# Kernel optimization log

Hardware: AMD Instinct MI355X
Metric: run time of the kernel (lower is better)

## Reference

```python
import jax, jax.numpy as jnp
import numpy as np

N_NODES = 100000
N_EDGES = 3200000
N_GRAPHS = 512
F_IN = 256
HID = 16
N_CLS = 8


def setup_inputs() -> dict:
    key = jax.random.key(0)
    ks = jax.random.split(key, 6)
    x = jax.random.normal(ks[0], (N_NODES, F_IN), jnp.float32)
    edge_index = jax.random.randint(ks[1], (2, N_EDGES), 0, N_NODES, dtype=jnp.int64)
    batch = jnp.sort(jax.random.randint(ks[2], (N_NODES,), 0, N_GRAPHS, dtype=jnp.int64))
    W1 = jax.random.normal(ks[3], (F_IN, HID), jnp.float32) / np.float32(np.sqrt(F_IN))
    b1 = jnp.zeros((HID,), jnp.float32)
    W2 = jax.random.normal(ks[4], (HID, N_CLS), jnp.float32) / np.float32(np.sqrt(HID))
    b2 = jnp.zeros((N_CLS,), jnp.float32)
    return {"x": x, "edge_index": edge_index, "batch": batch, "num_graphs": N_GRAPHS,
            "W1": W1, "b1": b1, "W2": W2, "b2": b2}


def _gcn_conv(x, src, dst, W, b, n):
    # PyG GCNConv: linear transform, then sym-normalized scatter-add (self-loops
    # already appended to src/dst by caller), bias added after aggregation.
    h = x @ W  # [N, out]
    deg = jax.ops.segment_sum(jnp.ones_like(dst, h.dtype), dst, num_segments=n)
    dinv = jax.lax.rsqrt(jnp.maximum(deg, 1.0))  # deg >= 1 due to self-loops
    norm = dinv[src] * dinv[dst]  # [E+N]
    out = jax.ops.segment_sum(h[src] * norm[:, None], dst, num_segments=n)
    return out + b


def reference(x, edge_index, batch, num_graphs, W1, b1, W2, b2):
    n = x.shape[0]
    loop = jnp.arange(n, dtype=edge_index.dtype)
    src = jnp.concatenate([edge_index[0], loop])
    dst = jnp.concatenate([edge_index[1], loop])
    h = jax.nn.relu(_gcn_conv(x, src, dst, W1, b1, n))
    h = _gcn_conv(h, src, dst, W2, b2, n)
    # global mean pool over graphs
    sums = jax.ops.segment_sum(h, batch, num_segments=num_graphs)
    cnt = jax.ops.segment_sum(jnp.ones((n,), h.dtype), batch, num_segments=num_graphs)
    return sums / jnp.maximum(cnt, 1.0)[:, None]
```

## Files before the change

kernel.cpp:

```cpp
#include <hip/hip_runtime.h>

#define F_IN 256
#define HID 16
#define NCLS 8
#define BSH 9
#define NPB 512
#define MAXBINS 256
#define BCAP 18432u
#define TILE 8192
#define WIN 8
#define GROWS 64
#define APITCH 280
#define BSPLIT 4

typedef float f4v __attribute__((ext_vector_type(4)));
typedef float f32x4 __attribute__((ext_vector_type(4)));
typedef _Float16 h2v __attribute__((ext_vector_type(2)));
typedef _Float16 f16x4 __attribute__((ext_vector_type(4)));
typedef _Float16 f16x8 __attribute__((ext_vector_type(8)));

__global__ void k_init(unsigned* __restrict__ binCur, int nbins,
                       const float* __restrict__ W1, _Float16* __restrict__ wfrag,
                       float* __restrict__ cg, int g,
                       float* __restrict__ out, int osz) {
    int t = threadIdx.x;
    if (t < nbins) binCur[t] = (unsigned)t * BCAP;
    if (t < 64) {
        int col = t & 15, k0 = (t >> 4) * 8;
#pragma unroll
        for (int kc = 0; kc < 8; ++kc) {
            f16x8 v;
#pragma unroll
            for (int j = 0; j < 8; ++j)
                v[j] = (_Float16)W1[(kc * 32 + k0 + j) * HID + col];
            *(f16x8*)&wfrag[((size_t)t * 8 + kc) * 8] = v;
        }
    }
    for (int i = t; i < g; i += 256) cg[i] = 0.f;
    for (int i = t; i < osz; i += 256) out[i] = 0.f;
}

__global__ void __launch_bounds__(512) k_binA(const int* __restrict__ src,
                                              const int* __restrict__ dst, int e,
                                              unsigned* __restrict__ binCur,
                                              unsigned* __restrict__ binbuf) {
    __shared__ unsigned scnt[MAXBINS], lbase[MAXBINS], gbase[MAXBINS];
    __shared__ unsigned sbuf[TILE];
    __shared__ unsigned char sbin[TILE];
    int t = threadIdx.x;
    if (t < MAXBINS) scnt[t] = 0u;
    __syncthreads();
    int base = blockIdx.x * TILE;
    unsigned ent[16], rank[16];
    int ebin[16];
#pragma unroll
    for (int i = 0; i < 16; ++i) {
        int j = base + t + i * 512;
        ebin[i] = -1;
        if (j < e) {
            int d = __builtin_nontemporal_load(&dst[j]);
            int s = __builtin_nontemporal_load(&src[j]);
            ent[i] = ((unsigned)s << BSH) | ((unsigned)d & (NPB - 1));
            ebin[i] = d >> BSH;
            rank[i] = atomicAdd(&scnt[ebin[i]], 1u);
        }
    }
    __syncthreads();
    if (t == 0) {
        unsigned run = 0;
        for (int b = 0; b < MAXBINS; ++b) { lbase[b] = run; run += scnt[b]; }
    }
    __syncthreads();
    if (t < MAXBINS && scnt[t] > 0u) gbase[t] = atomicAdd(&binCur[t], scnt[t]);
    __syncthreads();
#pragma unroll
    for (int i = 0; i < 16; ++i)
        if (ebin[i] >= 0) {
            unsigned p = lbase[ebin[i]] + rank[i];
            sbuf[p] = ent[i];
            sbin[p] = (unsigned char)ebin[i];
        }
    __syncthreads();
    int total = e - base; if (total > TILE) total = TILE;
    for (int idx = t; idx < total; idx += 512) {
        int b = sbin[idx];
        __builtin_nontemporal_store(sbuf[idx], &binbuf[gbase[b] + ((unsigned)idx - lbase[b])]);
    }
}

__global__ void __launch_bounds__(256) k_binB1(const unsigned* __restrict__ binbuf,
                                               const unsigned* __restrict__ binCur,
                                               unsigned* __restrict__ phist) {
    __shared__ unsigned hist[NPB];
    int t = threadIdx.x;
    int b = blockIdx.x >> 2, sp = blockIdx.x & 3;
    unsigned base = (unsigned)b * BCAP;
    unsigned cnt = binCur[b] - base;
    unsigned q = cnt / BSPLIT;
    unsigned j0 = sp * q, j1 = (sp == BSPLIT - 1) ? cnt : j0 + q;
    for (int i = t; i < NPB; i += 256) hist[i] = 0u;
    __syncthreads();
    for (unsigned j = j0 + t; j < j1; j += 256)
        atomicAdd(&hist[__builtin_nontemporal_load(&binbuf[base + j]) & (NPB - 1)], 1u);
    __syncthreads();
    unsigned* ph = phist + ((size_t)b * BSPLIT + sp) * NPB;
    for (int i = t; i < NPB; i += 256) ph[i] = hist[i];
}

__global__ void __launch_bounds__(256) k_binB2(unsigned* __restrict__ phist, int n,
                                               unsigned* __restrict__ off,
                                               unsigned* __restrict__ degc) {
    __shared__ unsigned deg[NPB];
    __shared__ unsigned pref[NPB];
    __shared__ unsigned s1[256];
    int t = threadIdx.x;
    int b = blockIdx.x;
    unsigned* ph = phist + (size_t)b * BSPLIT * NPB;
    for (int i = t; i < NPB; i += 256) {
        unsigned c0 = ph[i], c1 = ph[NPB + i], c2 = ph[2 * NPB + i], c3 = ph[3 * NPB + i];
        ph[i] = 0u; ph[NPB + i] = c0; ph[2 * NPB + i] = c0 + c1; ph[3 * NPB + i] = c0 + c1 + c2;
        deg[i] = c0 + c1 + c2 + c3;
    }
    __syncthreads();
    unsigned h0 = deg[2 * t], h1 = deg[2 * t + 1];
    unsigned pair = h0 + h1;
    s1[t] = pair;
    __syncthreads();
    for (int o = 1; o < 256; o <<= 1) {
        unsigned v = (t >= o) ? s1[t - o] : 0u;
        __syncthreads();
        s1[t] += v;
        __syncthreads();
    }
    unsigned exc = s1[t] - pair;
    pref[2 * t] = exc;
    pref[2 * t + 1] = exc + h0;
    __syncthreads();
    unsigned base = (unsigned)b * BCAP;
    int dbase = b << BSH;
    for (int i = t; i < NPB; i += 256) {
        int d = dbase + i;
        if (d < n) { off[d] = base + pref[i]; degc[d] = deg[i]; }
    }
}

__global__ void __launch_bounds__(256) k_binB3(const unsigned* __restrict__ binbuf,
                                               const unsigned* __restrict__ binCur,
                                               const unsigned* __restrict__ phist,
                                               const unsigned* __restrict__ off,
                                               int n, unsigned* __restrict__ srcs) {
    __shared__ unsigned cst[NPB], cur[NPB], offl[NPB];
    int t = threadIdx.x;
    int b = blockIdx.x >> 2, sp = blockIdx.x & 3;
    unsigned base = (unsigned)b * BCAP;
    unsigned cnt = binCur[b] - base;
    unsigned q = cnt / BSPLIT;
    unsigned j0 = sp * q, j1 = (sp == BSPLIT - 1) ? cnt : j0 + q;
    const unsigned* ph = phist + ((size_t)b * BSPLIT + sp) * NPB;
    int dbase = b << BSH;
    for (int i = t; i < NPB; i += 256) {
        cst[i] = ph[i];
        cur[i] = 0u;
        int d = dbase + i;
        offl[i] = (d < n) ? off[d] : 0u;
    }
    __syncthreads();
    for (unsigned j = j0 + t; j < j1; j += 256) {
        unsigned v = __builtin_nontemporal_load(&binbuf[base + j]);
        unsigned dl = v & (NPB - 1);
        unsigned r = atomicAdd(&cur[dl], 1u);
        srcs[offl[dl] + cst[dl] + r] = v >> BSH;
    }
}

__global__ void __launch_bounds__(256) k_gemm1(const float* __restrict__ x,
                                               const _Float16* __restrict__ wfrag,
                                               const unsigned* __restrict__ degc,
                                               _Float16* __restrict__ t1h, int n) {
    __shared__ _Float16 xs[4][16 * APITCH];
    int t = threadIdx.x;
    int lane = t & 63;
    int wv = t >> 6;
    int col = lane & 15;
    int k0 = (lane >> 4) * 8;
    f16x8 bfrag[8];
#pragma unroll
    for (int kc = 0; kc < 8; ++kc)
        bfrag[kc] = *(const f16x8*)&wfrag[((size_t)lane * 8 + kc) * 8];
    int rbase = blockIdx.x * GROWS;
    int nrows = n - rbase; if (nrows > GROWS) nrows = GROWS;
#pragma unroll
    for (int it = 0; it < GROWS * 64 / 256; ++it) {
        int q = t + it * 256;
        int row = q >> 6, c4 = q & 63;
        if (row < nrows) {
            f4v v = __builtin_nontemporal_load(
                &((const f4v*)(x + (size_t)(rbase + row) * F_IN))[c4]);
            f16x4 hv;
            hv[0] = (_Float16)v[0]; hv[1] = (_Float16)v[1];
            hv[2] = (_Float16)v[2]; hv[3] = (_Float16)v[3];
            *(f16x4*)&xs[row >> 4][(row & 15) * APITCH + c4 * 4] = hv;
        }
    }
    __syncthreads();
    f32x4 acc = {0.f, 0.f, 0.f, 0.f};
    const _Float16* tile = xs[wv];
    int arow = lane & 15;
#pragma unroll
    for (int kc = 0; kc < 8; ++kc) {
        f16x8 afrag = *(const f16x8*)&tile[arow * APITCH + kc * 32 + k0];
        acc = __builtin_amdgcn_mfma_f32_16x16x32_f16(afrag, bfrag[kc], acc, 0, 0, 0);
    }
    int r0 = (lane >> 4) * 4;
#pragma unroll
    for (int reg = 0; reg < 4; ++reg) {
        int grow = rbase + wv * 16 + r0 + reg;
        if (grow < n) {
            float v = acc[reg] * rsqrtf((float)(degc[grow] + 1u));
            t1h[(size_t)grow * HID + col] = (_Float16)v;
        }
    }
}

__global__ void __launch_bounds__(256) k_agg1g2(const unsigned* __restrict__ srcs,
                                                const unsigned* __restrict__ off,
                                                const unsigned* __restrict__ degc,
                                                const uint2* __restrict__ t1q,
                                                const float* __restrict__ b1,
                                                const float* __restrict__ W2,
                                                unsigned* __restrict__ t2h, int n) {
    __shared__ float w2s[HID * NCLS];
    __shared__ float b1s[HID];
    int t = threadIdx.x;
    if (t < HID * NCLS) w2s[t] = W2[t];
    if (t < HID) b1s[t] = b1[t];
    __syncthreads();
    int d = blockIdx.x * 32 + (t >> 3);
    if (d >= n) return;
    int q4 = t & 3;
    int pr = (t >> 2) & 1;
    unsigned p = off[d];
    unsigned c = degc[d];
    float a0 = 0.f, a1 = 0.f, a2 = 0.f, a3 = 0.f;
    union { unsigned u; h2v h; } cv;
    unsigned i = pr;
    for (; i + 14 < c; i += 16) {
        unsigned s0 = srcs[p + i],      s1 = srcs[p + i + 2];
        unsigned s2 = srcs[p + i + 4],  s3 = srcs[p + i + 6];
        unsigned s4 = srcs[p + i + 8],  s5 = srcs[p + i + 10];
        unsigned s6 = srcs[p + i + 12], s7 = srcs[p + i + 14];
        uint2 w0 = t1q[(size_t)s0 * 4 + q4];
        uint2 w1 = t1q[(size_t)s1 * 4 + q4];
        uint2 w2 = t1q[(size_t)s2 * 4 + q4];
        uint2 w3 = t1q[(size_t)s3 * 4 + q4];
        uint2 w4 = t1q[(size_t)s4 * 4 + q4];
        uint2 w5 = t1q[(size_t)s5 * 4 + q4];
        uint2 w6 = t1q[(size_t)s6 * 4 + q4];
        uint2 w7 = t1q[(size_t)s7 * 4 + q4];
        cv.u = w0.x; a0 += (float)cv.h[0]; a1 += (float)cv.h[1];
        cv.u = w0.y; a2 += (float)cv.h[0]; a3 += (float)cv.h[1];
        cv.u = w1.x; a0 += (float)cv.h[0]; a1 += (float)cv.h[1];
        cv.u = w1.y; a2 += (float)cv.h[0]; a3 += (float)cv.h[1];
        cv.u = w2.x; a0 += (float)cv.h[0]; a1 += (float)cv.h[1];
        cv.u = w2.y; a2 += (float)cv.h[0]; a3 += (float)cv.h[1];
        cv.u = w3.x; a0 += (float)cv.h[0]; a1 += (float)cv.h[1];
        cv.u = w3.y; a2 += (float)cv.h[0]; a3 += (float)cv.h[1];
        cv.u = w4.x; a0 += (float)cv.h[0]; a1 += (float)cv.h[1];
        cv.u = w4.y; a2 += (float)cv.h[0]; a3 += (float)cv.h[1];
        cv.u = w5.x; a0 += (float)cv.h[0]; a1 += (float)cv.h[1];
        cv.u = w5.y; a2 += (float)cv.h[0]; a3 += (float)cv.h[1];
        cv.u = w6.x; a0 += (float)cv.h[0]; a1 += (float)cv.h[1];
        cv.u = w6.y; a2 += (float)cv.h[0]; a3 += (float)cv.h[1];
        cv.u = w7.x; a0 += (float)cv.h[0]; a1 += (float)cv.h[1];
        cv.u = w7.y; a2 += (float)cv.h[0]; a3 += (float)cv.h[1];
    }
    for (; i + 6 < c; i += 8) {
        unsigned s0 = srcs[p + i],     s1 = srcs[p + i + 2];
        unsigned s2 = srcs[p + i + 4], s3 = srcs[p + i + 6];
        uint2 w0 = t1q[(size_t)s0 * 4 + q4];
        uint2 w1 = t1q[(size_t)s1 * 4 + q4];
        uint2 w2 = t1q[(size_t)s2 * 4 + q4];
        uint2 w3 = t1q[(size_t)s3 * 4 + q4];
        cv.u = w0.x; a0 += (float)cv.h[0]; a1 += (float)cv.h[1];
        cv.u = w0.y; a2 += (float)cv.h[0]; a3 += (float)cv.h[1];
        cv.u = w1.x; a0 += (float)cv.h[0]; a1 += (float)cv.h[1];
        cv.u = w1.y; a2 += (float)cv.h[0]; a3 += (float)cv.h[1];
        cv.u = w2.x; a0 += (float)cv.h[0]; a1 += (float)cv.h[1];
        cv.u = w2.y; a2 += (float)cv.h[0]; a3 += (float)cv.h[1];
        cv.u = w3.x; a0 += (float)cv.h[0]; a1 += (float)cv.h[1];
        cv.u = w3.y; a2 += (float)cv.h[0]; a3 += (float)cv.h[1];
    }
    for (; i + 2 < c; i += 4) {
        uint2 w0 = t1q[(size_t)srcs[p + i] * 4 + q4];
        uint2 w1 = t1q[(size_t)srcs[p + i + 2] * 4 + q4];
        cv.u = w0.x; a0 += (float)cv.h[0]; a1 += (float)cv.h[1];
        cv.u = w0.y; a2 += (float)cv.h[0]; a3 += (float)cv.h[1];
        cv.u = w1.x; a0 += (float)cv.h[0]; a1 += (float)cv.h[1];
        cv.u = w1.y; a2 += (float)cv.h[0]; a3 += (float)cv.h[1];
    }
    if (i < c) {
        uint2 w = t1q[(size_t)srcs[p + i] * 4 + q4];
        cv.u = w.x; a0 += (float)cv.h[0]; a1 += (float)cv.h[1];
        cv.u = w.y; a2 += (float)cv.h[0]; a3 += (float)cv.h[1];
    }
    a0 += __shfl_xor(a0, 4, 64);
    a1 += __shfl_xor(a1, 4, 64);
    a2 += __shfl_xor(a2, 4, 64);
    a3 += __shfl_xor(a3, 4, 64);
    uint2 sl = t1q[(size_t)d * 4 + q4];
    cv.u = sl.x; a0 += (float)cv.h[0]; a1 += (float)cv.h[1];
    cv.u = sl.y; a2 += (float)cv.h[0]; a3 += (float)cv.h[1];
    float di = rsqrtf((float)(c + 1u));
    float h0 = fmaxf(di * a0 + b1s[4 * q4 + 0], 0.f);
    float h1 = fmaxf(di * a1 + b1s[4 * q4 + 1], 0.f);
    float h2 = fmaxf(di * a2 + b1s[4 * q4 + 2], 0.f);
    float h3 = fmaxf(di * a3 + b1s[4 * q4 + 3], 0.f);
    float o[NCLS];
#pragma unroll
    for (int cc = 0; cc < NCLS; ++cc)
        o[cc] = h0 * w2s[(4 * q4 + 0) * NCLS + cc] + h1 * w2s[(4 * q4 + 1) * NCLS + cc]
              + h2 * w2s[(4 * q4 + 2) * NCLS + cc] + h3 * w2s[(4 * q4 + 3) * NCLS + cc];
#pragma unroll
    for (int m = 1; m < 4; m <<= 1)
#pragma unroll
        for (int cc = 0; cc < NCLS; ++cc)
            o[cc] += __shfl_xor(o[cc], m, 64);
    if (pr == 0) {
        union { unsigned u; h2v h; } pk;
        pk.h[0] = (_Float16)(o[2 * q4] * di);
        pk.h[1] = (_Float16)(o[2 * q4 + 1] * di);
        t2h[(size_t)d * 4 + q4] = pk.u;
    }
}

__global__ void __launch_bounds__(256) k_agg2pool(const unsigned* __restrict__ srcs,
                                                  const unsigned* __restrict__ off,
                                                  const unsigned* __restrict__ degc,
                                                  const uint2* __restrict__ t2q,
                                                  const float* __restrict__ b2,
                                                  const int* __restrict__ batch,
                                                  float* __restrict__ out,
                                                  float* __restrict__ cg, int n) {
    __shared__ float wacc[WIN * NCLS];
    __shared__ float wcnt[WIN];
    __shared__ int gb_s;
    int t = threadIdx.x;
    int bbase = blockIdx.x * 64;
    if (t < WIN * NCLS) wacc[t] = 0.f;
    if (t < WIN) wcnt[t] = 0.f;
    if (t == 0) gb_s = batch[bbase < n ? bbase : (n - 1)];
    __syncthreads();
    int d = bbase + (t >> 2);
    int q2 = t & 1;
    int pr = (t >> 1) & 1;
    if (d < n) {
        unsigned p = off[d];
        unsigned c = degc[d];
        float a0 = 0.f, a1 = 0.f, a2 = 0.f, a3 = 0.f;
        union { unsigned u; h2v h; } cv;
        unsigned i = pr;
        for (; i + 14 < c; i += 16) {
            uint2 w0 = t2q[(size_t)srcs[p + i] * 2 + q2];
            uint2 w1 = t2q[(size_t)srcs[p + i + 2] * 2 + q2];
            uint2 w2 = t2q[(size_t)srcs[p + i + 4] * 2 + q2];
            uint2 w3 = t2q[(size_t)srcs[p + i + 6] * 2 + q2];
            uint2 w4 = t2q[(size_t)srcs[p + i + 8] * 2 + q2];
            uint2 w5 = t2q[(size_t)srcs[p + i + 10] * 2 + q2];
            uint2 w6 = t2q[(size_t)srcs[p + i + 12] * 2 + q2];
            uint2 w7 = t2q[(size_t)srcs[p + i + 14] * 2 + q2];
            cv.u = w0.x; a0 += (float)cv.h[0]; a1 += (float)cv.h[1];
            cv.u = w0.y; a2 += (float)cv.h[0]; a3 += (float)cv.h[1];
            cv.u = w1.x; a0 += (float)cv.h[0]; a1 += (float)cv.h[1];
            cv.u = w1.y; a2 += (float)cv.h[0]; a3 += (float)cv.h[1];
            cv.u = w2.x; a0 += (float)cv.h[0]; a1 += (float)cv.h[1];
            cv.u = w2.y; a2 += (float)cv.h[0]; a3 += (float)cv.h[1];
            cv.u = w3.x; a0 += (float)cv.h[0]; a1 += (float)cv.h[1];
            cv.u = w3.y; a2 += (float)cv.h[0]; a3 += (float)cv.h[1];
            cv.u = w4.x; a0 += (float)cv.h[0]; a1 += (float)cv.h[1];
            cv.u = w4.y; a2 += (float)cv.h[0]; a3 += (float)cv.h[1];
            cv.u = w5.x; a0 += (float)cv.h[0]; a1 += (float)cv.h[1];
            cv.u = w5.y; a2 += (float)cv.h[0]; a3 += (float)cv.h[1];
            cv.u = w6.x; a0 += (float)cv.h[0]; a1 += (float)cv.h[1];
            cv.u = w6.y; a2 += (float)cv.h[0]; a3 += (float)cv.h[1];
            cv.u = w7.x; a0 += (float)cv.h[0]; a1 += (float)cv.h[1];
            cv.u = w7.y; a2 += (float)cv.h[0]; a3 += (float)cv.h[1];
        }
        for (; i + 6 < c; i += 8) {
            uint2 w0 = t2q[(size_t)srcs[p + i] * 2 + q2];
            uint2 w1 = t2q[(size_t)srcs[p + i + 2] * 2 + q2];
            uint2 w2 = t2q[(size_t)srcs[p + i + 4] * 2 + q2];
            uint2 w3 = t2q[(size_t)srcs[p + i + 6] * 2 + q2];
            cv.u = w0.x; a0 += (float)cv.h[0]; a1 += (float)cv.h[1];
            cv.u = w0.y; a2 += (float)cv.h[0]; a3 += (float)cv.h[1];
            cv.u = w1.x; a0 += (float)cv.h[0]; a1 += (float)cv.h[1];
            cv.u = w1.y; a2 += (float)cv.h[0]; a3 += (float)cv.h[1];
            cv.u = w2.x; a0 += (float)cv.h[0]; a1 += (float)cv.h[1];
            cv.u = w2.y; a2 += (float)cv.h[0]; a3 += (float)cv.h[1];
            cv.u = w3.x; a0 += (float)cv.h[0]; a1 += (float)cv.h[1];
            cv.u = w3.y; a2 += (float)cv.h[0]; a3 += (float)cv.h[1];
        }
        for (; i + 2 < c; i += 4) {
            uint2 w0 = t2q[(size_t)srcs[p + i] * 2 + q2];
            uint2 w1 = t2q[(size_t)srcs[p + i + 2] * 2 + q2];
            cv.u = w0.x; a0 += (float)cv.h[0]; a1 += (float)cv.h[1];
            cv.u = w0.y; a2 += (float)cv.h[0]; a3 += (float)cv.h[1];
            cv.u = w1.x; a0 += (float)cv.h[0]; a1 += (float)cv.h[1];
            cv.u = w1.y; a2 += (float)cv.h[0]; a3 += (float)cv.h[1];
        }
        if (i < c) {
            uint2 w = t2q[(size_t)srcs[p + i] * 2 + q2];
            cv.u = w.x; a0 += (float)cv.h[0]; a1 += (float)cv.h[1];
            cv.u = w.y; a2 += (float)cv.h[0]; a3 += (float)cv.h[1];
        }
        a0 += __shfl_xor(a0, 2, 64);
        a1 += __shfl_xor(a1, 2, 64);
        a2 += __shfl_xor(a2, 2, 64);
        a3 += __shfl_xor(a3, 2, 64);
        if (pr == 0) {
            uint2 sl = t2q[(size_t)d * 2 + q2];
            cv.u = sl.x; a0 += (float)cv.h[0]; a1 += (float)cv.h[1];
            cv.u = sl.y; a2 += (float)cv.h[0]; a3 += (float)cv.h[1];
            float di = rsqrtf((float)(c + 1u));
            int f0 = 4 * q2;
            float v0 = di * a0 + b2[f0 + 0];
            float v1 = di * a1 + b2[f0 + 1];
            float v2 = di * a2 + b2[f0 + 2];
            float v3 = di * a3 + b2[f0 + 3];
            int g = batch[d];
            int gi = g - gb_s;
            if (gi < WIN) {
                atomicAdd(&wacc[gi * NCLS + f0 + 0], v0);
                atomicAdd(&wacc[gi * NCLS + f0 + 1], v1);
                atomicAdd(&wacc[gi * NCLS + f0 + 2], v2);
                atomicAdd(&wacc[gi * NCLS + f0 + 3], v3);
                if ((t & 3) == 0) atomicAdd(&wcnt[gi], 1.f);
            } else {
                atomicAdd(&out[(size_t)g * NCLS + f0 + 0], v0);
                atomicAdd(&out[(size_t)g * NCLS + f0 + 1], v1);
                atomicAdd(&out[(size_t)g * NCLS + f0 + 2], v2);
                atomicAdd(&out[(size_t)g * NCLS + f0 + 3], v3);
                if ((t & 3) == 0) atomicAdd(&cg[g], 1.f);
            }
        }
    }
    __syncthreads();
    if (t < WIN * NCLS && wcnt[t >> 3] > 0.f)
        atomicAdd(&out[(size_t)(gb_s + (t >> 3)) * NCLS + (t & 7)], wacc[t]);
    if (t < WIN && wcnt[t] > 0.f) atomicAdd(&cg[gb_s + t], wcnt[t]);
}

__global__ void k_div(float* __restrict__ out, const float* __restrict__ cg, int total) {
    int i = blockIdx.x * blockDim.x + threadIdx.x;
    if (i < total) out[i] /= fmaxf(cg[i / NCLS], 1.0f);
}

extern "C" void kernel_launch(void* const* d_in, const int* in_sizes, int n_in,
                              void* d_out, int out_size, void* d_ws, size_t ws_size,
                              hipStream_t stream) {
    const float* x = (const float*)d_in[0];
    const int* ei = (const int*)d_in[1];
    const int* batch = (const int*)d_in[2];
    const float* W1 = (const float*)d_in[4];
    const float* b1 = (const float*)d_in[5];
    const float* W2 = (const float*)d_in[6];
    const float* b2 = (const float*)d_in[7];

    int n = in_sizes[0] / F_IN;
    int e = in_sizes[1] / 2;
    int g = out_size / NCLS;
    const int* src = ei;
    const int* dst = ei + e;
    int nbins = (n + NPB - 1) >> BSH;

    char* w = (char*)d_ws;
    unsigned* binCur = (unsigned*)w; w += (size_t)MAXBINS * 4;
    unsigned* degc   = (unsigned*)w; w += (size_t)n * 4;
    unsigned* off    = (unsigned*)w; w += (size_t)n * 4;
    unsigned* t1h    = (unsigned*)w; w += (size_t)n * 8 * 4;
    unsigned* t2h    = (unsigned*)w; w += (size_t)n * 4 * 4;
    _Float16* wfrag  = (_Float16*)w; w += (size_t)64 * 8 * 8 * 2;
    float* cg        = (float*)w;    w += (size_t)g * 4;
    w = (char*)(((size_t)w + 255) & ~(size_t)255);
    unsigned* binbuf = (unsigned*)w; w += (size_t)nbins * BCAP * 4;
    unsigned* srcs   = (unsigned*)w; w += (size_t)nbins * BCAP * 4;
    unsigned* phist  = (unsigned*)w; w += (size_t)nbins * BSPLIT * NPB * 4;

    k_init<<<1, 256, 0, stream>>>(binCur, nbins, W1, wfrag, cg, g, (float*)d_out, out_size);
    k_binA<<<(e + TILE - 1) / TILE, 512, 0, stream>>>(src, dst, e, binCur, binbuf);
    k_binB1<<<nbins * BSPLIT, 256, 0, stream>>>(binbuf, binCur, phist);
    k_binB2<<<nbins, 256, 0, stream>>>(phist, n, off, degc);
    k_binB3<<<nbins * BSPLIT, 256, 0, stream>>>(binbuf, binCur, phist, off, n, srcs);
    k_gemm1<<<(n + GROWS - 1) / GROWS, 256, 0, stream>>>(x, wfrag, degc, (_Float16*)t1h, n);
    k_agg1g2<<<(n + 31) / 32, 256, 0, stream>>>(srcs, off, degc, (const uint2*)t1h,
                                                b1, W2, t2h, n);
    k_agg2pool<<<(n + 63) / 64, 256, 0, stream>>>(srcs, off, degc, (const uint2*)t2h,
                                                  b2, batch, (float*)d_out, cg, n);
    k_div<<<(out_size + 255) / 256, 256, 0, stream>>>((float*)d_out, cg, out_size);
}
```

Before: 186.4 us.

## Fuse three bin-sort passes into one kernel staging bin in LDS

Replaces the split histogram, prefix and scatter kernels (each with 4-way bin splits and a global partial-histogram buffer) with a single kernel per bin. Each block loads its bin's entries into a 72 KB LDS buffer once, builds the histogram, does the prefix scan, then scatters from LDS. This removes the second global read of binbuf, the phist traffic and two launches. In exchange it uses only one block per bin (about 196 blocks) with large LDS, which lowers parallelism and occupancy.

```diff
diff --git a/kernel.cpp b/kernel.cpp
--- a/kernel.cpp
+++ b/kernel.cpp
@@ -11,7 +11,6 @@
 #define WIN 8
 #define GROWS 64
 #define APITCH 280
-#define BSPLIT 4
 
 typedef float f4v __attribute__((ext_vector_type(4)));
 typedef float f32x4 __attribute__((ext_vector_type(4)));
@@ -88,41 +87,29 @@
     }
 }
 
-__global__ void __launch_bounds__(256) k_binB1(const unsigned* __restrict__ binbuf,
-                                               const unsigned* __restrict__ binCur,
-                                               unsigned* __restrict__ phist) {
+__global__ void __launch_bounds__(256) k_binB(const unsigned* __restrict__ binbuf,
+                                              const unsigned* __restrict__ binCur,
+                                              int n,
+                                              unsigned* __restrict__ srcs,
+                                              unsigned* __restrict__ off,
+                                              unsigned* __restrict__ degc) {
+    __shared__ unsigned sbuf[BCAP];
     __shared__ unsigned hist[NPB];
-    int t = threadIdx.x;
-    int b = blockIdx.x >> 2, sp = blockIdx.x & 3;
+    __shared__ unsigned pref[NPB];
+    __shared__ unsigned s1[256];
+    int t = threadIdx.x;
+    int b = blockIdx.x;
     unsigned base = (unsigned)b * BCAP;
     unsigned cnt = binCur[b] - base;
-    unsigned q = cnt / BSPLIT;
-    unsigned j0 = sp * q, j1 = (sp == BSPLIT - 1) ? cnt : j0 + q;
     for (int i = t; i < NPB; i += 256) hist[i] = 0u;
     __syncthreads();
-    for (unsigned j = j0 + t; j < j1; j += 256)
-        atomicAdd(&hist[__builtin_nontemporal_load(&binbuf[base + j]) & (NPB - 1)], 1u);
-    __syncthreads();
-    unsigned* ph = phist + ((size_t)b * BSPLIT + sp) * NPB;
-    for (int i = t; i < NPB; i += 256) ph[i] = hist[i];
-}
-
-__global__ void __launch_bounds__(256) k_binB2(unsigned* __restrict__ phist, int n,
-                                               unsigned* __restrict__ off,
-                                               unsigned* __restrict__ degc) {
-    __shared__ unsigned deg[NPB];
-    __shared__ unsigned pref[NPB];
-    __shared__ unsigned s1[256];
-    int t = threadIdx.x;
-    int b = blockIdx.x;
-    unsigned* ph = phist + (size_t)b * BSPLIT * NPB;
-    for (int i = t; i < NPB; i += 256) {
-        unsigned c0 = ph[i], c1 = ph[NPB + i], c2 = ph[2 * NPB + i], c3 = ph[3 * NPB + i];
-        ph[i] = 0u; ph[NPB + i] = c0; ph[2 * NPB + i] = c0 + c1; ph[3 * NPB + i] = c0 + c1 + c2;
-        deg[i] = c0 + c1 + c2 + c3;
-    }
-    __syncthreads();
-    unsigned h0 = deg[2 * t], h1 = deg[2 * t + 1];
+    for (unsigned j = t; j < cnt; j += 256) {
+        unsigned v = __builtin_nontemporal_load(&binbuf[base + j]);
+        sbuf[j] = v;
+        atomicAdd(&hist[v & (NPB - 1)], 1u);
+    }
+    __syncthreads();
+    unsigned h0 = hist[2 * t], h1 = hist[2 * t + 1];
     unsigned pair = h0 + h1;
     s1[t] = pair;
     __syncthreads();
@@ -136,40 +123,19 @@
     pref[2 * t] = exc;
     pref[2 * t + 1] = exc + h0;
     __syncthreads();
-    unsigned base = (unsigned)b * BCAP;
     int dbase = b << BSH;
     for (int i = t; i < NPB; i += 256) {
         int d = dbase + i;
-        if (d < n) { off[d] = base + pref[i]; degc[d] = deg[i]; }
-    }
-}
-
-__global__ void __launch_bounds__(256) k_binB3(const unsigned* __restrict__ binbuf,
-                                               const unsigned* __restrict__ binCur,
-                                               const unsigned* __restrict__ phist,
-                                               const unsigned* __restrict__ off,
-                                               int n, unsigned* __restrict__ srcs) {
-    __shared__ unsigned cst[NPB], cur[NPB], offl[NPB];
-    int t = threadIdx.x;
-    int b = blockIdx.x >> 2, sp = blockIdx.x & 3;
-    unsigned base = (unsigned)b * BCAP;
-    unsigned cnt = binCur[b] - base;
-    unsigned q = cnt / BSPLIT;
-    unsigned j0 = sp * q, j1 = (sp == BSPLIT - 1) ? cnt : j0 + q;
-    const unsigned* ph = phist + ((size_t)b * BSPLIT + sp) * NPB;
-    int dbase = b << BSH;
-    for (int i = t; i < NPB; i += 256) {
-        cst[i] = ph[i];
-        cur[i] = 0u;
-        int d = dbase + i;
-        offl[i] = (d < n) ? off[d] : 0u;
-    }
-    __syncthreads();
-    for (unsigned j = j0 + t; j < j1; j += 256) {
-        unsigned v = __builtin_nontemporal_load(&binbuf[base + j]);
+        if (d < n) { off[d] = base + pref[i]; degc[d] = hist[i]; }
+    }
+    __syncthreads();
+    for (int i = t; i < NPB; i += 256) hist[i] = 0u;
+    __syncthreads();
+    for (unsigned j = t; j < cnt; j += 256) {
+        unsigned v = sbuf[j];
         unsigned dl = v & (NPB - 1);
-        unsigned r = atomicAdd(&cur[dl], 1u);
-        srcs[offl[dl] + cst[dl] + r] = v >> BSH;
+        unsigned r = atomicAdd(&hist[dl], 1u);
+        srcs[base + pref[dl] + r] = v >> BSH;
     }
 }
 
@@ -483,13 +449,10 @@
     w = (char*)(((size_t)w + 255) & ~(size_t)255);
     unsigned* binbuf = (unsigned*)w; w += (size_t)nbins * BCAP * 4;
     unsigned* srcs   = (unsigned*)w; w += (size_t)nbins * BCAP * 4;
-    unsigned* phist  = (unsigned*)w; w += (size_t)nbins * BSPLIT * NPB * 4;
 
     k_init<<<1, 256, 0, stream>>>(binCur, nbins, W1, wfrag, cg, g, (float*)d_out, out_size);
     k_binA<<<(e + TILE - 1) / TILE, 512, 0, stream>>>(src, dst, e, binCur, binbuf);
-    k_binB1<<<nbins * BSPLIT, 256, 0, stream>>>(binbuf, binCur, phist);
-    k_binB2<<<nbins, 256, 0, stream>>>(phist, n, off, degc);
-    k_binB3<<<nbins * BSPLIT, 256, 0, stream>>>(binbuf, binCur, phist, off, n, srcs);
+    k_binB<<<nbins, 256, 0, stream>>>(binbuf, binCur, n, srcs, off, degc);
     k_gemm1<<<(n + GROWS - 1) / GROWS, 256, 0, stream>>>(x, wfrag, degc, (_Float16*)t1h, n);
     k_agg1g2<<<(n + 31) / 32, 256, 0, stream>>>(srcs, off, degc, (const uint2*)t1h,
                                                 b1, W2, t2h, n);
```

Measured after the change: 160.5 us, median of 2. 1.16x faster.
